# Optimization experiments

Measured on AMD Instinct MI355X. Metric: run time of the kernel, lower is better.

Reference implementation:

```python
import jax, jax.numpy as jnp
import numpy as np

HIDDEN = 4096
N_HEADS = 32
N_KV_HEADS = 8
HEAD_DIM = 128
ROPE_THETA = 1e6
RMS_EPS = 1e-6
SEQ = 2048


def setup_inputs() -> dict:
    key = jax.random.key(0)
    k1, k2, k3 = jax.random.split(key, 3)
    hidden_states = jax.random.normal(k1, (SEQ, HIDDEN), dtype=jnp.float32)
    # fused QKV weight: [hidden, (H + 2*Hkv) * head_dim]
    qkv_out = (N_HEADS + 2 * N_KV_HEADS) * HEAD_DIM
    w_qkv = jax.random.normal(k2, (HIDDEN, qkv_out), dtype=jnp.float32) * (HIDDEN ** -0.5)
    w_o = jax.random.normal(k3, (N_HEADS * HEAD_DIM, HIDDEN), dtype=jnp.float32) * ((N_HEADS * HEAD_DIM) ** -0.5)
    q_norm_w = jnp.ones((HEAD_DIM,), dtype=jnp.float32)
    k_norm_w = jnp.ones((HEAD_DIM,), dtype=jnp.float32)
    # NeoX-style rotary tables [T, head_dim/2]
    pos = jnp.arange(SEQ, dtype=jnp.float32)
    inv_freq = 1.0 / (ROPE_THETA ** (jnp.arange(0, HEAD_DIM, 2, dtype=jnp.float32) / HEAD_DIM))
    freqs = pos[:, None] * inv_freq[None, :]  # [T, d/2]
    cos = jnp.cos(freqs)
    sin = jnp.sin(freqs)
    return {"hidden_states": hidden_states, "cos": cos, "sin": sin,
            "w_qkv": w_qkv, "w_o": w_o, "q_norm_w": q_norm_w, "k_norm_w": k_norm_w}


def _rms_norm(x, w, eps=RMS_EPS):
    # per-head RMSNorm over last dim (head_dim)
    var = jnp.mean(jnp.square(x), axis=-1, keepdims=True)
    return x * jax.lax.rsqrt(var + eps) * w


def _rope(x, cos, sin):
    # NeoX rotate-half: x split into two halves of head_dim
    d2 = x.shape[-1] // 2
    x1, x2 = x[..., :d2], x[..., d2:]
    c = cos[:, None, :]  # [T,1,d/2] broadcast over heads
    s = sin[:, None, :]
    return jnp.concatenate([x1 * c - x2 * s, x2 * c + x1 * s], axis=-1)


def reference(hidden_states, cos, sin, w_qkv, w_o, q_norm_w, k_norm_w):
    T = hidden_states.shape[0]
    H, Hkv, D = N_HEADS, N_KV_HEADS, HEAD_DIM
    G = H // Hkv  # GQA group size
    scale = D ** -0.5

    qkv = hidden_states @ w_qkv  # [T, (H+2Hkv)*D]
    q, k, v = jnp.split(qkv, [H * D, (H + Hkv) * D], axis=1)
    q = q.reshape(T, H, D)
    k = k.reshape(T, Hkv, D)
    v = v.reshape(T, Hkv, D)

    q = _rms_norm(q, q_norm_w)
    k = _rms_norm(k, k_norm_w)
    q = _rope(q, cos, sin)
    k = _rope(k, cos, sin)

    # GQA: group query heads onto shared KV heads
    qg = q.reshape(T, Hkv, G, D)
    scores = jnp.einsum('qhgd,khd->hgqk', qg, k) * scale  # [Hkv,G,T,T]
    causal = jnp.tril(jnp.ones((T, T), dtype=bool))
    scores = jnp.where(causal, scores, jnp.float32(-1e30))
    probs = jax.nn.softmax(scores, axis=-1)
    out = jnp.einsum('hgqk,khd->qhgd', probs, v).reshape(T, H * D)
    return out @ w_o  # [T, hidden]
```

## Files before the change

### kernel.cpp

```cpp
#include <hip/hip_runtime.h>
#include <stdint.h>

#define SEQ   2048
#define HID   4096
#define NQH   32
#define NKVH  8
#define HD    128
#define QKVN  6144

typedef uint16_t u16;
typedef __attribute__((ext_vector_type(8))) short bf16x8;
typedef __attribute__((ext_vector_type(4))) float f32x4;
typedef __attribute__((ext_vector_type(4))) unsigned int u32x4;

static __device__ __forceinline__ float bf2f(u16 h){
  union { float f; unsigned int u; } v; v.u = ((unsigned int)h) << 16; return v.f;
}
static __device__ __forceinline__ u16 f2bf(float f){
  unsigned int u = __float_as_uint(f);
  return (u16)((u + 0x7fffu + ((u >> 16) & 1u)) >> 16);
}
static __device__ __forceinline__ f32x4 mfma16(bf16x8 a, bf16x8 b, f32x4 c){
  return __builtin_amdgcn_mfma_f32_16x16x32_bf16(a, b, c, 0, 0, 0);
}
static __device__ __forceinline__ void gload16(const void* g, void* l){
  __builtin_amdgcn_global_load_lds((const __attribute__((address_space(1))) void*)g,
                                   (__attribute__((address_space(3))) void*)l, 16, 0, 0);
}

__global__ void k_cvt(const float* __restrict__ src, u16* __restrict__ dst, int n4){
  int i = blockIdx.x * blockDim.x + threadIdx.x;
  if (i >= n4) return;
  float4 v = ((const float4*)src)[i];
  uint2 o;
  o.x = (unsigned)f2bf(v.x) | ((unsigned)f2bf(v.y) << 16);
  o.y = (unsigned)f2bf(v.z) | ((unsigned)f2bf(v.w) << 16);
  ((uint2*)dst)[i] = o;
}

__global__ void k_addf(const float* __restrict__ a, float* __restrict__ o, int n4){
  int i = blockIdx.x * blockDim.x + threadIdx.x;
  if (i >= n4) return;
  float4 x = ((const float4*)o)[i];
  float4 y = ((const float4*)a)[i];
  x.x += y.x; x.y += y.y; x.z += y.z; x.w += y.w;
  ((float4*)o)[i] = x;
}

__global__ void k_transpose_cvt(const float* __restrict__ src, u16* __restrict__ dst, int K, int N){
  __shared__ float t[32][33];
  int n0 = blockIdx.x * 32, k0 = blockIdx.y * 32;
  int tx = threadIdx.x, ty = threadIdx.y;
#pragma unroll
  for (int i = 0; i < 32; i += 8)
    t[ty + i][tx] = src[(size_t)(k0 + ty + i) * N + n0 + tx];
  __syncthreads();
#pragma unroll
  for (int i = 0; i < 32; i += 8)
    dst[(size_t)(n0 + ty + i) * K + k0 + tx] = f2bf(t[tx][ty + i]);
}

template<int OUTBF, int SPLITK, int XBC, int NBY>
__global__ __launch_bounds__(512) void k_gemm(const u16* __restrict__ A, const u16* __restrict__ Bt,
                                              void* __restrict__ Cv0, void* __restrict__ Cv1,
                                              int M, int N, int K){
  __shared__ __align__(16) u16 Asm[2][2][128][64];
  __shared__ __align__(16) u16 Bsm[2][2][128][64];
  const int tid = threadIdx.x, lane = tid & 63, wid = tid >> 6;
  const int wm = wid >> 2, wn = wid & 3;
  const int l16 = lane & 15, lhi = lane >> 4;
  const int rx = l16 & 7;
  const int bid = blockIdx.x;
  const int xcd = bid & 7, jj = bid >> 3;
  const int bcol_i = xcd * XBC + jj % XBC;
  const int rest = jj / XBC;
  const int brow_i = rest % NBY;
  const int kz = (SPLITK > 1) ? (rest / NBY) : 0;
  const size_t brow = (size_t)brow_i * 256, bcol = (size_t)bcol_i * 256;
  const int kbeg = kz * (K / SPLITK);
  void* Cv = (kz == 0) ? Cv0 : Cv1;

  const f32x4 vz = {0.f, 0.f, 0.f, 0.f};
  f32x4 acc[8][4];
#pragma unroll
  for (int m = 0; m < 8; m++)
#pragma unroll
    for (int n = 0; n < 4; n++) acc[m][n] = vz;

  const int srow = lane >> 3;
  const int sg   = (lane & 7) ^ srow;
  const u16* Ags = A  + (brow + wid*8 + srow) * (size_t)K + sg*8 + kbeg;
  const u16* Bgs = Bt + (bcol + wid*8 + srow) * (size_t)K + sg*8 + kbeg;
  const int NT = (K / SPLITK) >> 6;
  const int NU = NT >> 1;

#define FRA(buf, mi, kh) (*(const bf16x8*)&Asm[buf][wm][(mi)*16 + l16][(((kh)*4 + lhi) ^ rx) << 3])
#define FRB(buf, ni, kh) (*(const bf16x8*)&Bsm[buf][wn >> 1][(wn & 1)*64 + (ni)*16 + l16][(((kh)*4 + lhi) ^ rx) << 3])
#define STG_A(tile, half) do{ if ((tile) < NT){                                  \
    const size_t ko_ = (size_t)((half)*128) * K + (size_t)(tile) * 64;           \
    gload16(Ags + ko_,                &Asm[(tile)&1][half][wid*8][0]);           \
    gload16(Ags + ko_ + (size_t)64*K, &Asm[(tile)&1][half][64 + wid*8][0]); } }while(0)
#define STG_B(tile, half) do{ if ((tile) < NT){                                  \
    const size_t ko_ = (size_t)((half)*128) * K + (size_t)(tile) * 64;           \
    gload16(Bgs + ko_,                &Bsm[(tile)&1][half][wid*8][0]);           \
    gload16(Bgs + ko_ + (size_t)64*K, &Bsm[(tile)&1][half][64 + wid*8][0]); } }while(0)

  STG_B(0, 0); STG_B(0, 1); STG_A(0, 0); STG_A(0, 1); STG_B(1, 0); STG_B(1, 1);
  asm volatile("s_waitcnt vmcnt(4)" ::: "memory");
  __builtin_amdgcn_sched_barrier(0);
  __builtin_amdgcn_s_barrier();

  bf16x8 fA[4][2], fB01[2][2], fB23[2][2];
  for (int u = 0; u < NU; ++u){
    const int t = 2 * u;
#pragma unroll
    for (int mi = 0; mi < 4; ++mi){ fA[mi][0] = FRA(0, mi, 0); fA[mi][1] = FRA(0, mi, 1); }
#pragma unroll
    for (int ni = 0; ni < 2; ++ni){ fB01[ni][0] = FRB(0, ni, 0); fB01[ni][1] = FRB(0, ni, 1); }
    STG_A(t + 1, 0);
    asm volatile("s_waitcnt lgkmcnt(8)" ::: "memory");
    __builtin_amdgcn_s_barrier();
    asm volatile("s_waitcnt lgkmcnt(0)" ::: "memory");
    __builtin_amdgcn_sched_barrier(0);
    __builtin_amdgcn_s_setprio(1);
#pragma unroll
    for (int kh = 0; kh < 2; ++kh)
#pragma unroll
      for (int mi = 0; mi < 4; ++mi)
#pragma unroll
        for (int ni = 0; ni < 2; ++ni)
          acc[mi][ni] = mfma16(fA[mi][kh], fB01[ni][kh], acc[mi][ni]);
    __builtin_amdgcn_s_setprio(0);
    __builtin_amdgcn_s_barrier();
#pragma unroll
    for (int ni = 0; ni < 2; ++ni){ fB23[ni][0] = FRB(0, 2 + ni, 0); fB23[ni][1] = FRB(0, 2 + ni, 1); }
    STG_A(t + 1, 1);
    __builtin_amdgcn_s_barrier();
    asm volatile("s_waitcnt lgkmcnt(0)" ::: "memory");
    __builtin_amdgcn_sched_barrier(0);
    __builtin_amdgcn_s_setprio(1);
#pragma unroll
    for (int kh = 0; kh < 2; ++kh)
#pragma unroll
      for (int mi = 0; mi < 4; ++mi)
#pragma unroll
        for (int ni = 0; ni < 2; ++ni)
          acc[mi][2 + ni] = mfma16(fA[mi][kh], fB23[ni][kh], acc[mi][2 + ni]);
    __builtin_amdgcn_s_setprio(0);
    __builtin_amdgcn_s_barrier();
#pragma unroll
    for (int mi = 0; mi < 4; ++mi){ fA[mi][0] = FRA(0, 4 + mi, 0); fA[mi][1] = FRA(0, 4 + mi, 1); }
    STG_B(t + 2, 0);
    __builtin_amdgcn_s_barrier();
    asm volatile("s_waitcnt lgkmcnt(0)" ::: "memory");
    __builtin_amdgcn_sched_barrier(0);
    __builtin_amdgcn_s_setprio(1);
#pragma unroll
    for (int kh = 0; kh < 2; ++kh)
#pragma unroll
      for (int mi = 0; mi < 4; ++mi)
#pragma unroll
        for (int ni = 0; ni < 2; ++ni)
          acc[4 + mi][ni] = mfma16(fA[mi][kh], fB01[ni][kh], acc[4 + mi][ni]);
    __builtin_amdgcn_s_setprio(0);
    __builtin_amdgcn_s_barrier();
    STG_B(t + 2, 1);
    __builtin_amdgcn_s_barrier();
    asm volatile("s_waitcnt lgkmcnt(0)" ::: "memory");
    __builtin_amdgcn_sched_barrier(0);
    __builtin_amdgcn_s_setprio(1);
#pragma unroll
    for (int kh = 0; kh < 2; ++kh)
#pragma unroll
      for (int mi = 0; mi < 4; ++mi)
#pragma unroll
        for (int ni = 0; ni < 2; ++ni)
          acc[4 + mi][2 + ni] = mfma16(fA[mi][kh], fB23[ni][kh], acc[4 + mi][2 + ni]);
    __builtin_amdgcn_s_setprio(0);
    if (u == NU - 1) asm volatile("s_waitcnt vmcnt(0)" ::: "memory");
    else             asm volatile("s_waitcnt vmcnt(4)" ::: "memory");
    __builtin_amdgcn_sched_barrier(0);
    __builtin_amdgcn_s_barrier();
#pragma unroll
    for (int mi = 0; mi < 4; ++mi){ fA[mi][0] = FRA(1, mi, 0); fA[mi][1] = FRA(1, mi, 1); }
#pragma unroll
    for (int ni = 0; ni < 2; ++ni){ fB01[ni][0] = FRB(1, ni, 0); fB01[ni][1] = FRB(1, ni, 1); }
    STG_A(t + 2, 0);
    asm volatile("s_waitcnt lgkmcnt(8)" ::: "memory");
    __builtin_amdgcn_s_barrier();
    asm volatile("s_waitcnt lgkmcnt(0)" ::: "memory");
    __builtin_amdgcn_sched_barrier(0);
    __builtin_amdgcn_s_setprio(1);
#pragma unroll
    for (int kh = 0; kh < 2; ++kh)
#pragma unroll
      for (int mi = 0; mi < 4; ++mi)
#pragma unroll
        for (int ni = 0; ni < 2; ++ni)
          acc[mi][ni] = mfma16(fA[mi][kh], fB01[ni][kh], acc[mi][ni]);
    __builtin_amdgcn_s_setprio(0);
    __builtin_amdgcn_s_barrier();
#pragma unroll
    for (int ni = 0; ni < 2; ++ni){ fB23[ni][0] = FRB(1, 2 + ni, 0); fB23[ni][1] = FRB(1, 2 + ni, 1); }
    STG_A(t + 2, 1);
    __builtin_amdgcn_s_barrier();
    asm volatile("s_waitcnt lgkmcnt(0)" ::: "memory");
    __builtin_amdgcn_sched_barrier(0);
    __builtin_amdgcn_s_setprio(1);
#pragma unroll
    for (int kh = 0; kh < 2; ++kh)
#pragma unroll
      for (int mi = 0; mi < 4; ++mi)
#pragma unroll
        for (int ni = 0; ni < 2; ++ni)
          acc[mi][2 + ni] = mfma16(fA[mi][kh], fB23[ni][kh], acc[mi][2 + ni]);
    __builtin_amdgcn_s_setprio(0);
    __builtin_amdgcn_s_barrier();
#pragma unroll
    for (int mi = 0; mi < 4; ++mi){ fA[mi][0] = FRA(1, 4 + mi, 0); fA[mi][1] = FRA(1, 4 + mi, 1); }
    STG_B(t + 3, 0);
    __builtin_amdgcn_s_barrier();
    asm volatile("s_waitcnt lgkmcnt(0)" ::: "memory");
    __builtin_amdgcn_sched_barrier(0);
    __builtin_amdgcn_s_setprio(1);
#pragma unroll
    for (int kh = 0; kh < 2; ++kh)
#pragma unroll
      for (int mi = 0; mi < 4; ++mi)
#pragma unroll
        for (int ni = 0; ni < 2; ++ni)
          acc[4 + mi][ni] = mfma16(fA[mi][kh], fB01[ni][kh], acc[4 + mi][ni]);
    __builtin_amdgcn_s_setprio(0);
    __builtin_amdgcn_s_barrier();
    STG_B(t + 3, 1);
    __builtin_amdgcn_s_barrier();
    asm volatile("s_waitcnt lgkmcnt(0)" ::: "memory");
    __builtin_amdgcn_sched_barrier(0);
    __builtin_amdgcn_s_setprio(1);
#pragma unroll
    for (int kh = 0; kh < 2; ++kh)
#pragma unroll
      for (int mi = 0; mi < 4; ++mi)
#pragma unroll
        for (int ni = 0; ni < 2; ++ni)
          acc[4 + mi][2 + ni] = mfma16(fA[mi][kh], fB23[ni][kh], acc[4 + mi][2 + ni]);
    __builtin_amdgcn_s_setprio(0);
    asm volatile("s_waitcnt vmcnt(4)" ::: "memory");
    __builtin_amdgcn_sched_barrier(0);
    __builtin_amdgcn_s_barrier();
  }
#undef FRA
#undef FRB
#undef STG_A
#undef STG_B

#pragma unroll
  for (int mi = 0; mi < 8; mi++)
#pragma unroll
    for (int ni = 0; ni < 4; ni++)
#pragma unroll
      for (int i = 0; i < 4; i++){
        size_t row = brow + wm*128 + mi*16 + lhi*4 + i;
        size_t col = bcol + wn*64 + ni*16 + l16;
        if (OUTBF) ((u16*)Cv)[row * (size_t)N + col] = f2bf(acc[mi][ni][i]);
        else       ((float*)Cv)[row * (size_t)N + col] = acc[mi][ni][i];
      }
}

__global__ __launch_bounds__(256) void k_rmsrope(const u16* __restrict__ qkv, const float* __restrict__ cosp,
                                                 const float* __restrict__ sinp, const float* __restrict__ qw,
                                                 const float* __restrict__ kw, u16* __restrict__ Qr,
                                                 u16* __restrict__ Kr){
  int t = blockIdx.x;
  int lane = threadIdx.x & 63, w = threadIdx.x >> 6;
  int hh = blockIdx.y * 4 + w;
  bool isq = hh < NQH;
  int hl = isq ? hh : hh - NQH;
  const u16* src = qkv + (size_t)t * QKVN + (isq ? hl * HD : NQH * HD + hl * HD);
  unsigned u = *(const unsigned*)(src + 2 * lane);
  float x0 = bf2f((u16)(u & 0xffffu)), x1 = bf2f((u16)(u >> 16));
  float ss = x0 * x0 + x1 * x1;
#pragma unroll
  for (int m = 1; m < 64; m <<= 1) ss += __shfl_xor(ss, m);
  float rs = rsqrtf(ss * (1.f / HD) + 1e-6f);
  const float* wp = isq ? qw : kw;
  float w0 = wp[2 * lane], w1 = wp[2 * lane + 1];
  float xn0 = x0 * rs * w0, xn1 = x1 * rs * w1;
  float p0 = __shfl_xor(xn0, 32), p1 = __shfl_xor(xn1, 32);
  int j0 = (2 * lane) & 63;
  float c0 = cosp[t * 64 + j0], c1 = cosp[t * 64 + j0 + 1];
  float s0 = sinp[t * 64 + j0], s1 = sinp[t * 64 + j0 + 1];
  float o0, o1;
  if (lane < 32){ o0 = xn0 * c0 - p0 * s0; o1 = xn1 * c1 - p1 * s1; }
  else          { o0 = xn0 * c0 + p0 * s0; o1 = xn1 * c1 + p1 * s1; }
  if (isq){ o0 *= 0.08838834764831845f; o1 *= 0.08838834764831845f; }
  u16* dst = isq ? (Qr + ((size_t)hl * SEQ + t) * HD) : (Kr + ((size_t)hl * SEQ + t) * HD);
  *(unsigned*)(dst + 2 * lane) = (unsigned)f2bf(o0) | ((unsigned)f2bf(o1) << 16);
}

__global__ void k_vt(const u16* __restrict__ qkv, u16* __restrict__ VT){
  __shared__ u16 t[32][33];
  int t0 = blockIdx.x * 32, d0 = blockIdx.y * 32, hv = blockIdx.z;
  int tx = threadIdx.x, ty = threadIdx.y;
#pragma unroll
  for (int i = 0; i < 32; i += 8)
    t[ty + i][tx] = qkv[(size_t)(t0 + ty + i) * QKVN + (NQH + NKVH) * HD + hv * HD + d0 + tx];
  __syncthreads();
#pragma unroll
  for (int i = 0; i < 32; i += 8)
    VT[((size_t)hv * HD + d0 + ty + i) * SEQ + t0 + tx] = t[tx][ty + i];
}

__global__ __launch_bounds__(512) void k_attn(const u16* __restrict__ Q, const u16* __restrict__ Kg,
                                              const u16* __restrict__ VTg, u16* __restrict__ AO){
  __shared__ __align__(16) u16 Ksm[2][128][128];
  __shared__ __align__(16) u16 Vsm[128][128];
  __shared__ __align__(16) u16 Psm[8][16][136];
  int tid = threadIdx.x, lane = tid & 63, wid = tid >> 6;
  int l16 = lane & 15, lhi = lane >> 4;
  int bid = blockIdx.x;
  int kvg = bid & 7, rr = bid >> 3;
  int J = 15 - (rr >> 2);
  int hq = kvg * 4 + (rr & 3);
  int qb = J * 128;
  const u16* Kh = Kg  + (size_t)kvg * SEQ * HD;
  const u16* Vh = VTg + (size_t)kvg * HD * SEQ;
  const u16* Qh = Q   + (size_t)hq * SEQ * HD;

  bf16x8 qf[4];
#pragma unroll
  for (int ks = 0; ks < 4; ks++)
    qf[ks] = *(const bf16x8*)(Qh + (size_t)(qb + wid*16 + l16) * HD + ks*32 + lhi*8);

  const f32x4 vz = {0.f, 0.f, 0.f, 0.f};
  f32x4 o[8];
  float mrow[4], lrow[4];
#pragma unroll
  for (int n = 0; n < 8; n++) o[n] = vz;
#pragma unroll
  for (int i = 0; i < 4; i++){ mrow[i] = -1e30f; lrow[i] = 0.f; }

  int rsub = lane >> 4, g = lane & 15;
  const u16 *Ks0, *Ks1, *Ks2, *Ks3, *Vs0, *Vs1, *Vs2, *Vs3;
  {
    int r0 = wid*16 + 0*4 + rsub, r1 = wid*16 + 1*4 + rsub;
    int r2 = wid*16 + 2*4 + rsub, r3 = wid*16 + 3*4 + rsub;
    Ks0 = Kh + (size_t)r0 * HD + ((g ^ (r0 & 7)) << 3);
    Ks1 = Kh + (size_t)r1 * HD + ((g ^ (r1 & 7)) << 3);
    Ks2 = Kh + (size_t)r2 * HD + ((g ^ (r2 & 7)) << 3);
    Ks3 = Kh + (size_t)r3 * HD + ((g ^ (r3 & 7)) << 3);
    Vs0 = Vh + (size_t)r0 * SEQ + ((g ^ (r0 & 7)) << 3);
    Vs1 = Vh + (size_t)r1 * SEQ + ((g ^ (r1 & 7)) << 3);
    Vs2 = Vh + (size_t)r2 * SEQ + ((g ^ (r2 & 7)) << 3);
    Vs3 = Vh + (size_t)r3 * SEQ + ((g ^ (r3 & 7)) << 3);
  }

  gload16(Ks0, &Ksm[0][wid*16 +  0][0]);
  gload16(Ks1, &Ksm[0][wid*16 +  4][0]);
  gload16(Ks2, &Ksm[0][wid*16 +  8][0]);
  gload16(Ks3, &Ksm[0][wid*16 + 12][0]);
  asm volatile("s_waitcnt vmcnt(0)" ::: "memory");
  __builtin_amdgcn_sched_barrier(0);
  __builtin_amdgcn_s_barrier();

  int ntr = J + 1;
  int wrow0 = qb + wid*16;
  for (int t = 0; t < ntr; t++){
    int cur = t & 1, nxt = cur ^ 1;
    int kt0 = t << 7;
    bool pf = (t + 1 < ntr);
    gload16(Vs0 + kt0, &Vsm[wid*16 +  0][0]);
    gload16(Vs1 + kt0, &Vsm[wid*16 +  4][0]);
    gload16(Vs2 + kt0, &Vsm[wid*16 +  8][0]);
    gload16(Vs3 + kt0, &Vsm[wid*16 + 12][0]);
    if (pf){
      size_t ko = (size_t)(kt0 + 128) * HD;
      gload16(Ks0 + ko, &Ksm[nxt][wid*16 +  0][0]);
      gload16(Ks1 + ko, &Ksm[nxt][wid*16 +  4][0]);
      gload16(Ks2 + ko, &Ksm[nxt][wid*16 +  8][0]);
      gload16(Ks3 + ko, &Ksm[nxt][wid*16 + 12][0]);
    }
    f32x4 s[8];
#pragma unroll
    for (int n = 0; n < 8; n++) s[n] = vz;
    const u16* kbase = &Ksm[cur][0][0];
    __builtin_amdgcn_s_setprio(1);
#pragma unroll
    for (int n = 0; n < 8; n++){
      int row = n*16 + l16, rxk = row & 7;
#pragma unroll
      for (int ks = 0; ks < 4; ks++){
        bf16x8 kf = *(const bf16x8*)(kbase + row*128 + (((ks*4 + lhi) ^ rxk) << 3));
        s[n] = mfma16(qf[ks], kf, s[n]);
      }
    }
    __builtin_amdgcn_s_setprio(0);
    if (kt0 + 127 > wrow0){
#pragma unroll
      for (int n = 0; n < 8; n++)
#pragma unroll
        for (int i = 0; i < 4; i++)
          if (kt0 + n*16 + l16 > wrow0 + lhi*4 + i) s[n][i] = -1e30f;
    }
#pragma unroll
    for (int i = 0; i < 4; i++){
      float tm = fmaxf(fmaxf(fmaxf(s[0][i], s[1][i]), fmaxf(s[2][i], s[3][i])),
                       fmaxf(fmaxf(s[4][i], s[5][i]), fmaxf(s[6][i], s[7][i])));
      tm = fmaxf(tm, __shfl_xor(tm, 1));
      tm = fmaxf(tm, __shfl_xor(tm, 2));
      tm = fmaxf(tm, __shfl_xor(tm, 4));
      tm = fmaxf(tm, __shfl_xor(tm, 8));
      float nm = fmaxf(mrow[i], tm);
      float sc = __expf(mrow[i] - nm);
      mrow[i] = nm;
      float rsum = 0.f;
#pragma unroll
      for (int n = 0; n < 8; n++){
        float p = __expf(s[n][i] - nm);
        s[n][i] = p;
        rsum += p;
      }
      rsum += __shfl_xor(rsum, 1);
      rsum += __shfl_xor(rsum, 2);
      rsum += __shfl_xor(rsum, 4);
      rsum += __shfl_xor(rsum, 8);
      lrow[i] = lrow[i] * sc + rsum;
#pragma unroll
      for (int n = 0; n < 8; n++) o[n][i] *= sc;
    }
#pragma unroll
    for (int n = 0; n < 8; n++)
#pragma unroll
      for (int i = 0; i < 4; i++)
        Psm[wid][lhi*4 + i][n*16 + l16] = f2bf(s[n][i]);
    if (pf) asm volatile("s_waitcnt vmcnt(4)" ::: "memory");
    else    asm volatile("s_waitcnt vmcnt(0)" ::: "memory");
    __builtin_amdgcn_sched_barrier(0);
    __builtin_amdgcn_s_barrier();
    __builtin_amdgcn_sched_barrier(0);
    __builtin_amdgcn_s_setprio(1);
#pragma unroll
    for (int ksv = 0; ksv < 4; ksv++){
      bf16x8 pa = *(const bf16x8*)&Psm[wid][l16][ksv*32 + lhi*8];
#pragma unroll
      for (int n = 0; n < 8; n++){
        int row = n*16 + l16;
        bf16x8 vb = *(const bf16x8*)(&Vsm[0][0] + row*128 + (((ksv*4 + lhi) ^ (row & 7)) << 3));
        o[n] = mfma16(pa, vb, o[n]);
      }
    }
    __builtin_amdgcn_s_setprio(0);
    asm volatile("s_waitcnt vmcnt(0)" ::: "memory");
    __builtin_amdgcn_sched_barrier(0);
    __builtin_amdgcn_s_barrier();
  }
  float inv[4];
#pragma unroll
  for (int i = 0; i < 4; i++) inv[i] = 1.f / lrow[i];
#pragma unroll
  for (int n = 0; n < 8; n++)
#pragma unroll
    for (int i = 0; i < 4; i++){
      int trow = wrow0 + lhi*4 + i;
      AO[(size_t)trow * HID + hq * HD + n*16 + l16] = f2bf(o[n][i] * inv[i]);
    }
}

extern "C" void kernel_launch(void* const* d_in, const int* in_sizes, int n_in,
                              void* d_out, int out_size, void* d_ws, size_t ws_size,
                              hipStream_t stream){
  const float* hs   = (const float*)d_in[0];
  const float* cosp = (const float*)d_in[1];
  const float* sinp = (const float*)d_in[2];
  const float* wqkv = (const float*)d_in[3];
  const float* wo   = (const float*)d_in[4];
  const float* qw   = (const float*)d_in[5];
  const float* kw   = (const float*)d_in[6];
  float* out = (float*)d_out;
  char* ws = (char*)d_ws;
  u16* XB    = (u16*)(ws + 0);
  u16* WQKVT = (u16*)(ws + 16777216);
  u16* WOT   = (u16*)(ws + 0);
  float* SCR = (float*)(ws + 33554432);
  u16* QKV   = (u16*)(ws + 67108864);
  u16* QR    = (u16*)(ws + 92274688);
  u16* KR    = (u16*)(ws + 109051904);
  u16* VTB   = (u16*)(ws + 113246208);
  u16* AOB   = (u16*)(ws + 117440512);

  k_cvt<<<(SEQ * HID / 4 + 255) / 256, 256, 0, stream>>>(hs, XB, SEQ * HID / 4);
  k_transpose_cvt<<<dim3(QKVN / 32, HID / 32), dim3(32, 8), 0, stream>>>(wqkv, WQKVT, HID, QKVN);
  k_gemm<1, 1, 3, 8><<<192, 512, 0, stream>>>(XB, WQKVT, QKV, nullptr, SEQ, QKVN, HID);
  k_transpose_cvt<<<dim3(HID / 32, HID / 32), dim3(32, 8), 0, stream>>>(wo, WOT, HID, HID);
  k_rmsrope<<<dim3(SEQ, 10), 256, 0, stream>>>(QKV, cosp, sinp, qw, kw, QR, KR);
  k_vt<<<dim3(SEQ / 32, HD / 32, NKVH), dim3(32, 8), 0, stream>>>(QKV, VTB);
  k_attn<<<512, 512, 0, stream>>>(QR, KR, VTB, AOB);
  k_gemm<0, 2, 2, 8><<<256, 512, 0, stream>>>(AOB, WOT, out, SCR, SEQ, HID, HID);
  k_addf<<<SEQ * HID / 4 / 256, 256, 0, stream>>>(SCR, out, SEQ * HID / 4);
}
```

Before: 344.9 us.

## Retile QKV GEMM to 256x192 and replace split-K output GEMM with 128x128 tiles

The QKV projection GEMM moves from 256x256 tiles on 192 blocks to 256x192 tiles on 256 blocks, so every CU gets work. The output projection drops split-K, which needed a scratch buffer and a separate add kernel. It now uses a new 128x128-tile, 256-thread GEMM with 512 blocks that writes fp32 directly. The cost is less data reuse per tile and a simpler, less pipelined loop in the new kernel.

After: 331.9 us (median of 2 runs). -3.8%, faster.

```diff
diff --git a/kernel.cpp b/kernel.cpp
--- a/kernel.cpp
+++ b/kernel.cpp
@@ -38,15 +38,6 @@
   ((uint2*)dst)[i] = o;
 }
 
-__global__ void k_addf(const float* __restrict__ a, float* __restrict__ o, int n4){
-  int i = blockIdx.x * blockDim.x + threadIdx.x;
-  if (i >= n4) return;
-  float4 x = ((const float4*)o)[i];
-  float4 y = ((const float4*)a)[i];
-  x.x += y.x; x.y += y.y; x.z += y.z; x.w += y.w;
-  ((float4*)o)[i] = x;
-}
-
 __global__ void k_transpose_cvt(const float* __restrict__ src, u16* __restrict__ dst, int K, int N){
   __shared__ float t[32][33];
   int n0 = blockIdx.x * 32, k0 = blockIdx.y * 32;
@@ -60,57 +51,50 @@
     dst[(size_t)(n0 + ty + i) * K + k0 + tx] = f2bf(t[tx][ty + i]);
 }
 
-template<int OUTBF, int SPLITK, int XBC, int NBY>
-__global__ __launch_bounds__(512) void k_gemm(const u16* __restrict__ A, const u16* __restrict__ Bt,
-                                              void* __restrict__ Cv0, void* __restrict__ Cv1,
-                                              int M, int N, int K){
-  __shared__ __align__(16) u16 Asm[2][2][128][64];
-  __shared__ __align__(16) u16 Bsm[2][2][128][64];
+__global__ __launch_bounds__(512) void k_gemm192(const u16* __restrict__ A, const u16* __restrict__ Bt,
+                                                 u16* __restrict__ Cv, int M, int N, int K){
+  __shared__ __align__(16) u16 Asm[2][256][64];
+  __shared__ __align__(16) u16 Bsm[2][192][64];
   const int tid = threadIdx.x, lane = tid & 63, wid = tid >> 6;
   const int wm = wid >> 2, wn = wid & 3;
   const int l16 = lane & 15, lhi = lane >> 4;
   const int rx = l16 & 7;
   const int bid = blockIdx.x;
   const int xcd = bid & 7, jj = bid >> 3;
-  const int bcol_i = xcd * XBC + jj % XBC;
-  const int rest = jj / XBC;
-  const int brow_i = rest % NBY;
-  const int kz = (SPLITK > 1) ? (rest / NBY) : 0;
-  const size_t brow = (size_t)brow_i * 256, bcol = (size_t)bcol_i * 256;
-  const int kbeg = kz * (K / SPLITK);
-  void* Cv = (kz == 0) ? Cv0 : Cv1;
+  const size_t bcol = (size_t)(xcd * 4 + jj % 4) * 192;
+  const size_t brow = (size_t)((jj / 4) & 7) * 256;
 
   const f32x4 vz = {0.f, 0.f, 0.f, 0.f};
-  f32x4 acc[8][4];
+  f32x4 acc[8][3];
 #pragma unroll
   for (int m = 0; m < 8; m++)
 #pragma unroll
-    for (int n = 0; n < 4; n++) acc[m][n] = vz;
+    for (int n = 0; n < 3; n++) acc[m][n] = vz;
 
   const int srow = lane >> 3;
   const int sg   = (lane & 7) ^ srow;
-  const u16* Ags = A  + (brow + wid*8 + srow) * (size_t)K + sg*8 + kbeg;
-  const u16* Bgs = Bt + (bcol + wid*8 + srow) * (size_t)K + sg*8 + kbeg;
-  const int NT = (K / SPLITK) >> 6;
-  const int NU = NT >> 1;
-
-#define FRA(buf, mi, kh) (*(const bf16x8*)&Asm[buf][wm][(mi)*16 + l16][(((kh)*4 + lhi) ^ rx) << 3])
-#define FRB(buf, ni, kh) (*(const bf16x8*)&Bsm[buf][wn >> 1][(wn & 1)*64 + (ni)*16 + l16][(((kh)*4 + lhi) ^ rx) << 3])
+  const u16* Ags = A  + (brow + wid*8 + srow) * (size_t)K + sg*8;
+  const u16* Bgs = Bt + (bcol + wid*8 + srow) * (size_t)K + sg*8;
+  const int NT = K >> 6, NU = NT >> 1;
+
+#define FRA(buf, mi, kh) (*(const bf16x8*)&Asm[buf][wm*128 + (mi)*16 + l16][(((kh)*4 + lhi) ^ rx) << 3])
+#define FRB(buf, ni, kh) (*(const bf16x8*)&Bsm[buf][wn*48 + (ni)*16 + l16][(((kh)*4 + lhi) ^ rx) << 3])
 #define STG_A(tile, half) do{ if ((tile) < NT){                                  \
     const size_t ko_ = (size_t)((half)*128) * K + (size_t)(tile) * 64;           \
-    gload16(Ags + ko_,                &Asm[(tile)&1][half][wid*8][0]);           \
-    gload16(Ags + ko_ + (size_t)64*K, &Asm[(tile)&1][half][64 + wid*8][0]); } }while(0)
-#define STG_B(tile, half) do{ if ((tile) < NT){                                  \
-    const size_t ko_ = (size_t)((half)*128) * K + (size_t)(tile) * 64;           \
-    gload16(Bgs + ko_,                &Bsm[(tile)&1][half][wid*8][0]);           \
-    gload16(Bgs + ko_ + (size_t)64*K, &Bsm[(tile)&1][half][64 + wid*8][0]); } }while(0)
-
-  STG_B(0, 0); STG_B(0, 1); STG_A(0, 0); STG_A(0, 1); STG_B(1, 0); STG_B(1, 1);
-  asm volatile("s_waitcnt vmcnt(4)" ::: "memory");
+    gload16(Ags + ko_,                &Asm[(tile)&1][(half)*128 + wid*8][0]);     \
+    gload16(Ags + ko_ + (size_t)64*K, &Asm[(tile)&1][(half)*128 + 64 + wid*8][0]); } }while(0)
+#define STG_B(tile, r) do{ if ((tile) < NT){                                     \
+    const size_t ko_ = (size_t)((r)*64) * K + (size_t)(tile) * 64;               \
+    gload16(Bgs + ko_, &Bsm[(tile)&1][(r)*64 + wid*8][0]); } }while(0)
+
+  STG_B(0,0); STG_B(0,1); STG_B(0,2);
+  STG_A(0,0); STG_A(0,1);
+  STG_B(1,0); STG_B(1,1); STG_B(1,2);
+  asm volatile("s_waitcnt vmcnt(3)" ::: "memory");
   __builtin_amdgcn_sched_barrier(0);
   __builtin_amdgcn_s_barrier();
 
-  bf16x8 fA[4][2], fB01[2][2], fB23[2][2];
+  bf16x8 fA[4][2], fB01[2][2], fB2[2];
   for (int u = 0; u < NU; ++u){
     const int t = 2 * u;
 #pragma unroll
@@ -132,8 +116,7 @@
           acc[mi][ni] = mfma16(fA[mi][kh], fB01[ni][kh], acc[mi][ni]);
     __builtin_amdgcn_s_setprio(0);
     __builtin_amdgcn_s_barrier();
-#pragma unroll
-    for (int ni = 0; ni < 2; ++ni){ fB23[ni][0] = FRB(0, 2 + ni, 0); fB23[ni][1] = FRB(0, 2 + ni, 1); }
+    fB2[0] = FRB(0, 2, 0); fB2[1] = FRB(0, 2, 1);
     STG_A(t + 1, 1);
     __builtin_amdgcn_s_barrier();
     asm volatile("s_waitcnt lgkmcnt(0)" ::: "memory");
@@ -143,9 +126,7 @@
     for (int kh = 0; kh < 2; ++kh)
 #pragma unroll
       for (int mi = 0; mi < 4; ++mi)
-#pragma unroll
-        for (int ni = 0; ni < 2; ++ni)
-          acc[mi][2 + ni] = mfma16(fA[mi][kh], fB23[ni][kh], acc[mi][2 + ni]);
+        acc[mi][2] = mfma16(fA[mi][kh], fB2[kh], acc[mi][2]);
     __builtin_amdgcn_s_setprio(0);
     __builtin_amdgcn_s_barrier();
 #pragma unroll
@@ -164,21 +145,19 @@
           acc[4 + mi][ni] = mfma16(fA[mi][kh], fB01[ni][kh], acc[4 + mi][ni]);
     __builtin_amdgcn_s_setprio(0);
     __builtin_amdgcn_s_barrier();
-    STG_B(t + 2, 1);
-    __builtin_amdgcn_s_barrier();
-    asm volatile("s_waitcnt lgkmcnt(0)" ::: "memory");
-    __builtin_amdgcn_sched_barrier(0);
-    __builtin_amdgcn_s_setprio(1);
-#pragma unroll
-    for (int kh = 0; kh < 2; ++kh)
-#pragma unroll
-      for (int mi = 0; mi < 4; ++mi)
-#pragma unroll
-        for (int ni = 0; ni < 2; ++ni)
-          acc[4 + mi][2 + ni] = mfma16(fA[mi][kh], fB23[ni][kh], acc[4 + mi][2 + ni]);
+    STG_B(t + 2, 1); STG_B(t + 2, 2);
+    __builtin_amdgcn_s_barrier();
+    asm volatile("s_waitcnt lgkmcnt(0)" ::: "memory");
+    __builtin_amdgcn_sched_barrier(0);
+    __builtin_amdgcn_s_setprio(1);
+#pragma unroll
+    for (int kh = 0; kh < 2; ++kh)
+#pragma unroll
+      for (int mi = 0; mi < 4; ++mi)
+        acc[4 + mi][2] = mfma16(fA[mi][kh], fB2[kh], acc[4 + mi][2]);
     __builtin_amdgcn_s_setprio(0);
     if (u == NU - 1) asm volatile("s_waitcnt vmcnt(0)" ::: "memory");
-    else             asm volatile("s_waitcnt vmcnt(4)" ::: "memory");
+    else             asm volatile("s_waitcnt vmcnt(3)" ::: "memory");
     __builtin_amdgcn_sched_barrier(0);
     __builtin_amdgcn_s_barrier();
 #pragma unroll
@@ -200,8 +179,7 @@
           acc[mi][ni] = mfma16(fA[mi][kh], fB01[ni][kh], acc[mi][ni]);
     __builtin_amdgcn_s_setprio(0);
     __builtin_amdgcn_s_barrier();
-#pragma unroll
-    for (int ni = 0; ni < 2; ++ni){ fB23[ni][0] = FRB(1, 2 + ni, 0); fB23[ni][1] = FRB(1, 2 + ni, 1); }
+    fB2[0] = FRB(1, 2, 0); fB2[1] = FRB(1, 2, 1);
     STG_A(t + 2, 1);
     __builtin_amdgcn_s_barrier();
     asm volatile("s_waitcnt lgkmcnt(0)" ::: "memory");
@@ -211,9 +189,7 @@
     for (int kh = 0; kh < 2; ++kh)
 #pragma unroll
       for (int mi = 0; mi < 4; ++mi)
-#pragma unroll
-        for (int ni = 0; ni < 2; ++ni)
-          acc[mi][2 + ni] = mfma16(fA[mi][kh], fB23[ni][kh], acc[mi][2 + ni]);
+        acc[mi][2] = mfma16(fA[mi][kh], fB2[kh], acc[mi][2]);
     __builtin_amdgcn_s_setprio(0);
     __builtin_amdgcn_s_barrier();
 #pragma unroll
@@ -232,20 +208,18 @@
           acc[4 + mi][ni] = mfma16(fA[mi][kh], fB01[ni][kh], acc[4 + mi][ni]);
     __builtin_amdgcn_s_setprio(0);
     __builtin_amdgcn_s_barrier();
-    STG_B(t + 3, 1);
-    __builtin_amdgcn_s_barrier();
-    asm volatile("s_waitcnt lgkmcnt(0)" ::: "memory");
-    __builtin_amdgcn_sched_barrier(0);
-    __builtin_amdgcn_s_setprio(1);
-#pragma unroll
-    for (int kh = 0; kh < 2; ++kh)
-#pragma unroll
-      for (int mi = 0; mi < 4; ++mi)
-#pragma unroll
-        for (int ni = 0; ni < 2; ++ni)
-          acc[4 + mi][2 + ni] = mfma16(fA[mi][kh], fB23[ni][kh], acc[4 + mi][2 + ni]);
-    __builtin_amdgcn_s_setprio(0);
-    asm volatile("s_waitcnt vmcnt(4)" ::: "memory");
+    STG_B(t + 3, 1); STG_B(t + 3, 2);
+    __builtin_amdgcn_s_barrier();
+    asm volatile("s_waitcnt lgkmcnt(0)" ::: "memory");
+    __builtin_amdgcn_sched_barrier(0);
+    __builtin_amdgcn_s_setprio(1);
+#pragma unroll
+    for (int kh = 0; kh < 2; ++kh)
+#pragma unroll
+      for (int mi = 0; mi < 4; ++mi)
+        acc[4 + mi][2] = mfma16(fA[mi][kh], fB2[kh], acc[4 + mi][2]);
+    __builtin_amdgcn_s_setprio(0);
+    asm volatile("s_waitcnt vmcnt(3)" ::: "memory");
     __builtin_amdgcn_sched_barrier(0);
     __builtin_amdgcn_s_barrier();
   }
@@ -257,13 +231,106 @@
 #pragma unroll
   for (int mi = 0; mi < 8; mi++)
 #pragma unroll
-    for (int ni = 0; ni < 4; ni++)
+    for (int ni = 0; ni < 3; ni++)
 #pragma unroll
       for (int i = 0; i < 4; i++){
         size_t row = brow + wm*128 + mi*16 + lhi*4 + i;
+        size_t col = bcol + wn*48 + ni*16 + l16;
+        Cv[row * (size_t)N + col] = f2bf(acc[mi][ni][i]);
+      }
+}
+
+__global__ __launch_bounds__(256) void k_gemm128(const u16* __restrict__ A, const u16* __restrict__ Bt,
+                                                 float* __restrict__ Cv, int M, int N, int K){
+  __shared__ __align__(16) u16 Asm[2][128][64];
+  __shared__ __align__(16) u16 Bsm[2][128][64];
+  const int tid = threadIdx.x, lane = tid & 63, wid = tid >> 6;
+  const int wm = wid >> 1, wn = wid & 1;
+  const int l16 = lane & 15, lhi = lane >> 4;
+  const int rx = l16 & 7;
+  const int bid = blockIdx.x;
+  const int xcd = bid & 7, jj = bid >> 3;
+  const size_t bcol = (size_t)(xcd * 4 + (jj & 3)) * 128;
+  const size_t brow = (size_t)(jj >> 2) * 128;
+
+  const f32x4 vz = {0.f, 0.f, 0.f, 0.f};
+  f32x4 acc[4][4];
+#pragma unroll
+  for (int m = 0; m < 4; m++)
+#pragma unroll
+    for (int n = 0; n < 4; n++) acc[m][n] = vz;
+
+  const int srow = lane >> 3;
+  const int sg   = (lane & 7) ^ srow;
+  const u16* Ags = A  + (brow + wid*8 + srow) * (size_t)K + sg*8;
+  const u16* Bgs = Bt + (bcol + wid*8 + srow) * (size_t)K + sg*8;
+  const int NT = K >> 6;
+
+#define FRA2(buf, mi, kh) (*(const bf16x8*)&Asm[buf][wm*64 + (mi)*16 + l16][(((kh)*4 + lhi) ^ rx) << 3])
+#define FRB2(buf, ni, kh) (*(const bf16x8*)&Bsm[buf][wn*64 + (ni)*16 + l16][(((kh)*4 + lhi) ^ rx) << 3])
+#define STG2(tile) do{ if ((tile) < NT){                                          \
+    const size_t ko_ = (size_t)(tile) * 64;                                       \
+    _Pragma("unroll")                                                             \
+    for (int r_ = 0; r_ < 4; ++r_){                                               \
+      gload16(Ags + (size_t)(r_*32)*K + ko_, &Asm[(tile)&1][r_*32 + wid*8][0]);   \
+      gload16(Bgs + (size_t)(r_*32)*K + ko_, &Bsm[(tile)&1][r_*32 + wid*8][0]);   \
+    } } }while(0)
+
+  STG2(0);
+  asm volatile("s_waitcnt vmcnt(0)" ::: "memory");
+  __builtin_amdgcn_sched_barrier(0);
+  __builtin_amdgcn_s_barrier();
+
+  bf16x8 fa[4], fb[4];
+  for (int t = 0; t < NT; ++t){
+    const int cur = t & 1;
+    STG2(t + 1);
+#pragma unroll
+    for (int mi = 0; mi < 4; ++mi) fa[mi] = FRA2(cur, mi, 0);
+#pragma unroll
+    for (int ni = 0; ni < 4; ++ni) fb[ni] = FRB2(cur, ni, 0);
+    __builtin_amdgcn_s_barrier();
+    asm volatile("s_waitcnt lgkmcnt(0)" ::: "memory");
+    __builtin_amdgcn_sched_barrier(0);
+    __builtin_amdgcn_s_setprio(1);
+#pragma unroll
+    for (int mi = 0; mi < 4; ++mi)
+#pragma unroll
+      for (int ni = 0; ni < 4; ++ni)
+        acc[mi][ni] = mfma16(fa[mi], fb[ni], acc[mi][ni]);
+    __builtin_amdgcn_s_setprio(0);
+    __builtin_amdgcn_s_barrier();
+#pragma unroll
+    for (int mi = 0; mi < 4; ++mi) fa[mi] = FRA2(cur, mi, 1);
+#pragma unroll
+    for (int ni = 0; ni < 4; ++ni) fb[ni] = FRB2(cur, ni, 1);
+    __builtin_amdgcn_s_barrier();
+    asm volatile("s_waitcnt lgkmcnt(0)" ::: "memory");
+    __builtin_amdgcn_sched_barrier(0);
+    __builtin_amdgcn_s_setprio(1);
+#pragma unroll
+    for (int mi = 0; mi < 4; ++mi)
+#pragma unroll
+      for (int ni = 0; ni < 4; ++ni)
+        acc[mi][ni] = mfma16(fa[mi], fb[ni], acc[mi][ni]);
+    __builtin_amdgcn_s_setprio(0);
+    asm volatile("s_waitcnt vmcnt(0)" ::: "memory");
+    __builtin_amdgcn_sched_barrier(0);
+    __builtin_amdgcn_s_barrier();
+  }
+#undef FRA2
+#undef FRB2
+#undef STG2
+
+#pragma unroll
+  for (int mi = 0; mi < 4; mi++)
+#pragma unroll
+    for (int ni = 0; ni < 4; ni++)
+#pragma unroll
+      for (int i = 0; i < 4; i++){
+        size_t row = brow + wm*64 + mi*16 + lhi*4 + i;
         size_t col = bcol + wn*64 + ni*16 + l16;
-        if (OUTBF) ((u16*)Cv)[row * (size_t)N + col] = f2bf(acc[mi][ni][i]);
-        else       ((float*)Cv)[row * (size_t)N + col] = acc[mi][ni][i];
+        Cv[row * (size_t)N + col] = acc[mi][ni][i];
       }
 }
 
@@ -481,7 +548,6 @@
   u16* XB    = (u16*)(ws + 0);
   u16* WQKVT = (u16*)(ws + 16777216);
   u16* WOT   = (u16*)(ws + 0);
-  float* SCR = (float*)(ws + 33554432);
   u16* QKV   = (u16*)(ws + 67108864);
   u16* QR    = (u16*)(ws + 92274688);
   u16* KR    = (u16*)(ws + 109051904);
@@ -490,11 +556,10 @@
 
   k_cvt<<<(SEQ * HID / 4 + 255) / 256, 256, 0, stream>>>(hs, XB, SEQ * HID / 4);
   k_transpose_cvt<<<dim3(QKVN / 32, HID / 32), dim3(32, 8), 0, stream>>>(wqkv, WQKVT, HID, QKVN);
-  k_gemm<1, 1, 3, 8><<<192, 512, 0, stream>>>(XB, WQKVT, QKV, nullptr, SEQ, QKVN, HID);
+  k_gemm192<<<256, 512, 0, stream>>>(XB, WQKVT, QKV, SEQ, QKVN, HID);
   k_transpose_cvt<<<dim3(HID / 32, HID / 32), dim3(32, 8), 0, stream>>>(wo, WOT, HID, HID);
   k_rmsrope<<<dim3(SEQ, 10), 256, 0, stream>>>(QKV, cosp, sinp, qw, kw, QR, KR);
   k_vt<<<dim3(SEQ / 32, HD / 32, NKVH), dim3(32, 8), 0, stream>>>(QKV, VTB);
   k_attn<<<512, 512, 0, stream>>>(QR, KR, VTB, AOB);
-  k_gemm<0, 2, 2, 8><<<256, 512, 0, stream>>>(AOB, WOT, out, SCR, SEQ, HID, HID);
-  k_addf<<<SEQ * HID / 4 / 256, 256, 0, stream>>>(SCR, out, SEQ * HID / 4);
-}
+  k_gemm128<<<512, 256, 0, stream>>>(AOB, WOT, out, SEQ, HID, HID);
+}
```
